# Kernel optimization log

Measured on AMD Instinct MI355X. Metric: run time of the kernel, lower is better.

The kernel has to match this reference:

```python
import jax, jax.numpy as jnp
import numpy as np

B, T, F = 32, 64, 128          # batch, time_steps, input_dim
H = 8                           # feat_dim (GRU hidden, MHA embed)
NH, HD = 4, 2                   # num_heads, head_dim
HID = 32                        # hidden_dim (out_proj out-features)


def setup_inputs() -> dict:
    key = jax.random.key(0)
    ks = jax.random.split(key, 16)
    s = 0.1
    inp = {
        'x': jax.random.normal(ks[0], (B, T, F), jnp.float32),
        # input_proj: Linear(F, F)
        'Wp': jax.random.normal(ks[1], (F, F), jnp.float32) * s,
        'bp': jax.random.normal(ks[2], (F,), jnp.float32) * s,
        # per-feature GRU weights stacked over F (input size 1 -> squeeze)
        'W_ih': jax.random.normal(ks[3], (F, 3 * H), jnp.float32) * s,
        'b_ih': jax.random.normal(ks[4], (F, 3 * H), jnp.float32) * s,
        'W_hh': jax.random.normal(ks[5], (F, 3 * H, H), jnp.float32) * s,
        'b_hh': jax.random.normal(ks[6], (F, 3 * H), jnp.float32) * s,
        # shared MultiheadAttention (embed=H, heads=NH)
        'in_w': jax.random.normal(ks[7], (3 * H, H), jnp.float32) * s,
        'in_b': jax.random.normal(ks[8], (3 * H,), jnp.float32) * s,
        'ow': jax.random.normal(ks[9], (H, H), jnp.float32) * s,
        'ob': jax.random.normal(ks[10], (H,), jnp.float32) * s,
        # out_proj: Linear(F*H, HID)
        'Wout': jax.random.normal(ks[11], (HID, F * H), jnp.float32) * s,
        'bout': jax.random.normal(ks[12], (HID,), jnp.float32) * s,
    }
    return inp


def _forward(x, Wp, bp, W_ih, b_ih, W_hh, b_hh, in_w, in_b, ow, ob, Wout, bout):
    xp = x @ Wp.T + bp                               # [B,T,F] input_proj

    # ---- batched per-feature GRU (vectorized over B and F, scan over T) ----
    def step(h, x_t):                                # h [B,F,H], x_t [B,F]
        gx = x_t[..., None] * W_ih + b_ih            # [B,F,3H]
        gh = jnp.einsum('bfh,fgh->bfg', h, W_hh) + b_hh
        r = jax.nn.sigmoid(gx[..., :H] + gh[..., :H])
        z = jax.nn.sigmoid(gx[..., H:2 * H] + gh[..., H:2 * H])
        n = jnp.tanh(gx[..., 2 * H:] + r * gh[..., 2 * H:])
        h_new = (1.0 - z) * n + z * h
        return h_new, h_new

    h0 = jnp.zeros((x.shape[0], F, H), x.dtype)
    _, hs = jax.lax.scan(step, h0, jnp.moveaxis(xp, 1, 0))   # [T,B,F,H]
    out = jnp.moveaxis(hs, 0, 1)                              # [B,T,F,H]

    # ---- shared MHA over time, batched across (B, F) ----
    seq = out.transpose(0, 2, 1, 3)                           # [B,F,T,H]
    qkv = seq @ in_w.T + in_b                                 # [B,F,T,3H]
    q, k, v = jnp.split(qkv, 3, axis=-1)
    def heads(t):  # [B,F,T,H] -> [B,F,T,NH,HD]
        return t.reshape(t.shape[:-1] + (NH, HD))
    q, k, v = heads(q), heads(k), heads(v)
    scale = 1.0 / np.sqrt(HD)
    scores = jnp.einsum('bfqnd,bfknd->bfnqk', q, k) * scale   # [B,F,NH,T,T]
    w = jax.nn.softmax(scores, axis=-1)
    ctx = jnp.einsum('bfnqk,bfknd->bfqnd', w, v)
    ctx = ctx.reshape(ctx.shape[:2] + (ctx.shape[2], H))      # [B,F,T,H]
    attn_out = ctx @ ow.T + ob                                # [B,F,T,H]
    attention = attn_out.transpose(0, 2, 1, 3)                # [B,T,F,H]

    # ---- flatten GRU outputs and project ----
    y = out.reshape(out.shape[0], out.shape[1], F * H) @ Wout.T + bout  # [B,T,HID]
    return y, attention


def reference(x, Wp, bp, W_ih, b_ih, W_hh, b_hh, in_w, in_b, ow, ob, Wout, bout):
    return _forward(x, Wp, bp, W_ih, b_ih, W_hh, b_hh, in_w, in_b, ow, ob, Wout, bout)
```

## Files before the change

kernel.cpp:

```cpp
#include <hip/hip_runtime.h>


namespace {
constexpr int Bb = 32, Tt = 64, Ff = 128, Hh = 8, HIDh = 32;
constexpr int G3H = 24;
constexpr int XS_STRIDE = 130;
constexpr int XP_OFF = Tt * XS_STRIDE;
constexpr int SMEM_AB = XP_OFF + 8 * 65;
constexpr float L2E = 1.44269504088896340736f;
}

__device__ __forceinline__ float rcp_(float x) {
#if __has_builtin(__builtin_amdgcn_rcpf)
  return __builtin_amdgcn_rcpf(x);
#else
  return 1.0f / x;
#endif
}
__device__ __forceinline__ float exp2_(float x) {
#if __has_builtin(__builtin_amdgcn_exp2f)
  return __builtin_amdgcn_exp2f(x);
#else
  return exp2f(x);
#endif
}

__global__ __launch_bounds__(256) void k_gruproj(
    const float* __restrict__ x, const float* __restrict__ Wp, const float* __restrict__ bp,
    const float* __restrict__ W_ih, const float* __restrict__ b_ih,
    const float* __restrict__ W_hh, const float* __restrict__ b_hh,
    float* __restrict__ outp) {
  __shared__ float smem[SMEM_AB];
  const int tid = threadIdx.x;
  const int blk = blockIdx.x;
  const int b = blk >> 4;
  const int f0 = (blk & 15) * 8;
  const int lane = tid & 63;
  const int w = tid >> 6;

  {
    const float2* xb = (const float2*)(x + b * Tt * Ff);
    for (int i = tid; i < Tt * Ff / 2; i += 256) {
      int row = i >> 6, col2 = i & 63;
      *(float2*)&smem[row * XS_STRIDE + col2 * 2] = xb[i];
    }
  }
  __syncthreads();
  {
    const int t = lane;
    const int fA = f0 + w, fB = f0 + w + 4;
    float acc0 = bp[fA], acc1 = bp[fB];
    const float* wA = Wp + fA * Ff;
    const float* wB = Wp + fB * Ff;
    const float* xr = &smem[t * XS_STRIDE];
#pragma unroll 8
    for (int k = 0; k < Ff; k += 2) {
      float2 xv = *(const float2*)&xr[k];
      acc0 = fmaf(xv.x, wA[k], acc0); acc0 = fmaf(xv.y, wA[k + 1], acc0);
      acc1 = fmaf(xv.x, wB[k], acc1); acc1 = fmaf(xv.y, wB[k + 1], acc1);
    }
    smem[XP_OFF + w * 65 + t] = acc0;
    smem[XP_OFF + (w + 4) * 65 + t] = acc1;
  }
  __syncthreads();
  if (tid >= 64) return;

  {
    const int g = tid >> 3, j = tid & 7;
    const int f = f0 + g;
    const float* wb = W_hh + (f * G3H + j) * Hh;
    const float nL = -L2E, S2 = 2.0f * L2E;
    float w0s[8], w1s[8], w2s[8];
#pragma unroll
    for (int h = 0; h < 8; ++h) {
      w0s[h] = wb[h] * nL;
      w1s[h] = wb[64 + h] * nL;
      w2s[h] = wb[128 + h] * S2;
    }
    const float wi0s = W_ih[f * G3H + j] * nL;
    const float wi1s = W_ih[f * G3H + 8 + j] * nL;
    const float wi2s = W_ih[f * G3H + 16 + j] * S2;
    const float bias_r = (b_ih[f * G3H + j] + b_hh[f * G3H + j]) * nL;
    const float bias_z = (b_ih[f * G3H + 8 + j] + b_hh[f * G3H + 8 + j]) * nL;
    const float bi2s = b_ih[f * G3H + 16 + j] * S2;
    const float bh2s = b_hh[f * G3H + 16 + j] * S2;
    float hall[8];
#pragma unroll
    for (int h = 0; h < 8; ++h) hall[h] = 0.f;
    const int base = tid & 56;
    float* outb = outp + ((b * Ff + f) * Tt) * Hh + j;
    const float* xps = &smem[XP_OFF + g * 65];
    for (int t = 0; t < Tt; ++t) {
      float xt = xps[t];
      float a0 = bias_r, a1 = bias_z, a2 = bh2s;
#pragma unroll
      for (int h = 0; h < 8; ++h) {
        a0 = fmaf(hall[h], w0s[h], a0);
        a1 = fmaf(hall[h], w1s[h], a1);
        a2 = fmaf(hall[h], w2s[h], a2);
      }
      float r = rcp_(1.0f + exp2_(fmaf(xt, wi0s, a0)));
      float z = rcp_(1.0f + exp2_(fmaf(xt, wi1s, a1)));
      float narg = fmaf(r, a2, fmaf(xt, wi2s, bi2s));
      float n = fmaf(-2.0f, rcp_(exp2_(narg) + 1.0f), 1.0f);
      float hn = fmaf(z, hall[j] - n, n);
      outb[t * Hh] = hn;
#pragma unroll
      for (int h = 0; h < 8; ++h) hall[h] = __shfl(hn, base + h, 64);
    }
  }
}

__global__ __launch_bounds__(64) void k_mha(
    const float* __restrict__ outp, const float* __restrict__ in_w,
    const float* __restrict__ in_b, const float* __restrict__ ow,
    const float* __restrict__ ob, float* __restrict__ attn) {
  __shared__ float kvs[4 * 130];
  __shared__ float vvs[4 * 130];
  __shared__ float qs[64 * 10];
  __shared__ float cs[64 * 10];
  const int blk = blockIdx.x;
  const int b = blk >> 7, f = blk & 127;
  const int t = threadIdx.x;

  const float4* src = (const float4*)(outp + blk * (Tt * Hh));
  float4 r0 = src[t * 2], r1 = src[t * 2 + 1];
  float sq[8] = {r0.x, r0.y, r0.z, r0.w, r1.x, r1.y, r1.z, r1.w};
  constexpr float SCL = 0.70710678118654752f * L2E;
  float qv[8], ka[8], va[8];
#pragma unroll
  for (int jj = 0; jj < 8; ++jj) {
    float aq = in_b[jj], ak = in_b[8 + jj], av = in_b[16 + jj];
#pragma unroll
    for (int h = 0; h < 8; ++h) {
      aq = fmaf(sq[h], in_w[jj * 8 + h], aq);
      ak = fmaf(sq[h], in_w[(8 + jj) * 8 + h], ak);
      av = fmaf(sq[h], in_w[(16 + jj) * 8 + h], av);
    }
    qv[jj] = aq * SCL; ka[jj] = ak; va[jj] = av;
  }
#pragma unroll
  for (int n = 0; n < 4; ++n) {
    *(float2*)&qs[t * 10 + 2 * n] = make_float2(qv[2 * n], qv[2 * n + 1]);
    *(float2*)&kvs[n * 130 + 2 * t] = make_float2(ka[2 * n], ka[2 * n + 1]);
    *(float2*)&vvs[n * 130 + 2 * t] = make_float2(va[2 * n], va[2 * n + 1]);
  }
  __syncthreads();

  const int n = t & 3, qq = t >> 2;
  float q0[4], q1[4];
#pragma unroll
  for (int i = 0; i < 4; ++i) {
    float2 qp = *(const float2*)&qs[(qq + 16 * i) * 10 + 2 * n];
    q0[i] = qp.x; q1[i] = qp.y;
  }
  float ps[4], c0[4], c1[4];
#pragma unroll
  for (int i = 0; i < 4; ++i) { ps[i] = 0.f; c0[i] = 0.f; c1[i] = 0.f; }
#pragma unroll 4
  for (int kt = 0; kt < Tt; ++kt) {
    float2 kf = *(const float2*)&kvs[n * 130 + 2 * kt];
    float2 vf = *(const float2*)&vvs[n * 130 + 2 * kt];
#pragma unroll
    for (int i = 0; i < 4; ++i) {
      float s = fmaf(q0[i], kf.x, q1[i] * kf.y);
      float p = exp2_(s);
      ps[i] += p;
      c0[i] = fmaf(p, vf.x, c0[i]);
      c1[i] = fmaf(p, vf.y, c1[i]);
    }
  }
#pragma unroll
  for (int i = 0; i < 4; ++i) {
    float inv = rcp_(ps[i]);
    *(float2*)&cs[(qq + 16 * i) * 10 + 2 * n] = make_float2(c0[i] * inv, c1[i] * inv);
  }
  __syncthreads();

  const float4* owp = (const float4*)(ow + n * 16);
  float4 wv0 = owp[0], wv1 = owp[1], wv2 = owp[2], wv3 = owp[3];
  const float ob0 = ob[2 * n], ob1 = ob[2 * n + 1];
#pragma unroll
  for (int i = 0; i < 4; ++i) {
    int row = qq + 16 * i;
    float2 cp0 = *(const float2*)&cs[row * 10 + 0];
    float2 cp1 = *(const float2*)&cs[row * 10 + 2];
    float2 cp2 = *(const float2*)&cs[row * 10 + 4];
    float2 cp3 = *(const float2*)&cs[row * 10 + 6];
    float o0 = ob0, o1 = ob1;
    o0 = fmaf(cp0.x, wv0.x, o0); o0 = fmaf(cp0.y, wv0.y, o0);
    o0 = fmaf(cp1.x, wv0.z, o0); o0 = fmaf(cp1.y, wv0.w, o0);
    o0 = fmaf(cp2.x, wv1.x, o0); o0 = fmaf(cp2.y, wv1.y, o0);
    o0 = fmaf(cp3.x, wv1.z, o0); o0 = fmaf(cp3.y, wv1.w, o0);
    o1 = fmaf(cp0.x, wv2.x, o1); o1 = fmaf(cp0.y, wv2.y, o1);
    o1 = fmaf(cp1.x, wv2.z, o1); o1 = fmaf(cp1.y, wv2.w, o1);
    o1 = fmaf(cp2.x, wv3.x, o1); o1 = fmaf(cp2.y, wv3.y, o1);
    o1 = fmaf(cp3.x, wv3.z, o1); o1 = fmaf(cp3.y, wv3.w, o1);
    *(float2*)&attn[((b * Tt + row) * Ff + f) * Hh + 2 * n] = make_float2(o0, o1);
  }
}

__global__ __launch_bounds__(128) void k_outproj(
    const float* __restrict__ outp, const float* __restrict__ Wout,
    const float* __restrict__ bout, float* __restrict__ y) {
  constexpr int TT = 8;
  int blk = blockIdx.x;
  int b = blk >> 3;
  int t0 = (blk & 7) * TT;
  int tid = threadIdx.x;
  int oq = tid >> 4;
  int fc = tid & 15;
  float acc[TT][4];
#pragma unroll
  for (int tt = 0; tt < TT; ++tt)
#pragma unroll
    for (int od = 0; od < 4; ++od) acc[tt][od] = 0.f;
#pragma unroll
  for (int ff = 0; ff < 8; ++ff) {
    int f = fc * 8 + ff;
    const float4* rb = (const float4*)(outp + ((b * Ff + f) * Tt + t0) * Hh);
    float4 rv[16];
#pragma unroll
    for (int i = 0; i < 16; ++i) rv[i] = rb[i];
#pragma unroll
    for (int od = 0; od < 4; ++od) {
      int o = oq * 4 + od;
      const float4* wbp = (const float4*)(Wout + o * (Ff * Hh) + f * Hh);
      float4 wa = wbp[0], wc = wbp[1];
#pragma unroll
      for (int tt = 0; tt < TT; ++tt) {
        float4 ra = rv[tt * 2], rc = rv[tt * 2 + 1];
        float s = acc[tt][od];
        s = fmaf(ra.x, wa.x, s); s = fmaf(ra.y, wa.y, s);
        s = fmaf(ra.z, wa.z, s); s = fmaf(ra.w, wa.w, s);
        s = fmaf(rc.x, wc.x, s); s = fmaf(rc.y, wc.y, s);
        s = fmaf(rc.z, wc.z, s); s = fmaf(rc.w, wc.w, s);
        acc[tt][od] = s;
      }
    }
  }
#pragma unroll
  for (int tt = 0; tt < TT; ++tt)
#pragma unroll
    for (int od = 0; od < 4; ++od) {
      float v = acc[tt][od];
      v += __shfl_xor(v, 1, 16);
      v += __shfl_xor(v, 2, 16);
      v += __shfl_xor(v, 4, 16);
      v += __shfl_xor(v, 8, 16);
      acc[tt][od] = v;
    }
#pragma unroll
  for (int tt = 0; tt < TT; ++tt) {
    if (fc == tt) {
#pragma unroll
      for (int od = 0; od < 4; ++od) {
        int o = oq * 4 + od;
        y[(b * Tt + t0 + tt) * HIDh + o] = acc[tt][od] + bout[o];
      }
    }
  }
}

extern "C" void kernel_launch(void* const* d_in, const int* in_sizes, int n_in,
                              void* d_out, int out_size, void* d_ws, size_t ws_size,
                              hipStream_t stream) {
  (void)in_sizes; (void)n_in; (void)out_size; (void)ws_size;
  const float* x    = (const float*)d_in[0];
  const float* Wp   = (const float*)d_in[1];
  const float* bp   = (const float*)d_in[2];
  const float* W_ih = (const float*)d_in[3];
  const float* b_ih = (const float*)d_in[4];
  const float* W_hh = (const float*)d_in[5];
  const float* b_hh = (const float*)d_in[6];
  const float* in_w = (const float*)d_in[7];
  const float* in_b = (const float*)d_in[8];
  const float* ow   = (const float*)d_in[9];
  const float* ob   = (const float*)d_in[10];
  const float* Wout = (const float*)d_in[11];
  const float* bout = (const float*)d_in[12];

  float* y    = (float*)d_out;
  float* attn = (float*)d_out + Bb * Tt * HIDh;
  float* outp = (float*)d_ws;

  hipLaunchKernelGGL(k_gruproj, dim3(Bb * (Ff / 8)), dim3(256), 0, stream,
                     x, Wp, bp, W_ih, b_ih, W_hh, b_hh, outp);
  hipLaunchKernelGGL(k_mha, dim3(Bb * Ff), dim3(64), 0, stream,
                     outp, in_w, in_b, ow, ob, attn);
  hipLaunchKernelGGL(k_outproj, dim3(Bb * (Tt / 8)), dim3(128), 0, stream,
                     outp, Wout, bout, y);
}
```

Measured before the change: 64.31 us.

## Split input projection from GRU, merge MHA and out-projection into one launch

Moves the input projection out of the GRU kernel into its own kernel over all (b,t) rows, so the GRU kernel runs with 64-thread blocks and no longer carries 192 idle threads through the serial recurrence. Fuses the MHA and out-projection kernels into one launch: MHA blocks handle two (b,f) pairs each and the out-projection work is appended as extra blocks. Pads the K/V shared-memory layout to float4 per key. This trades an extra global round trip for xp and a new launch against better GRU occupancy and overlap between the MHA and out-projection work.

```diff
diff --git a/kernel.cpp b/kernel.cpp
--- a/kernel.cpp
+++ b/kernel.cpp
@@ -4,10 +4,12 @@
 namespace {
 constexpr int Bb = 32, Tt = 64, Ff = 128, Hh = 8, HIDh = 32;
 constexpr int G3H = 24;
-constexpr int XS_STRIDE = 130;
-constexpr int XP_OFF = Tt * XS_STRIDE;
-constexpr int SMEM_AB = XP_OFF + 8 * 65;
 constexpr float L2E = 1.44269504088896340736f;
+constexpr int KV4 = 0;
+constexpr int VV4 = 1040;
+constexpr int QS  = 2080;
+constexpr int CS  = 2720;
+constexpr int HALF = 3360;
 }
 
 __device__ __forceinline__ float rcp_(float x) {
@@ -25,238 +27,228 @@
 #endif
 }
 
-__global__ __launch_bounds__(256) void k_gruproj(
-    const float* __restrict__ x, const float* __restrict__ Wp, const float* __restrict__ bp,
-    const float* __restrict__ W_ih, const float* __restrict__ b_ih,
-    const float* __restrict__ W_hh, const float* __restrict__ b_hh,
-    float* __restrict__ outp) {
-  __shared__ float smem[SMEM_AB];
+__global__ __launch_bounds__(256) void k_inproj(
+    const float* __restrict__ x, const float* __restrict__ Wp,
+    const float* __restrict__ bp, float* __restrict__ xp) {
+  __shared__ float xs[2][128];
+  const int r0 = blockIdx.x * 2;
+  const int rr = threadIdx.x >> 7;
+  const int f = threadIdx.x & 127;
+  xs[rr][f] = x[(r0 + rr) * Ff + f];
+  __syncthreads();
+  float acc = bp[f];
+  const float4* wr = (const float4*)(Wp + f * Ff);
+  const float* xr = xs[rr];
+#pragma unroll 8
+  for (int k4 = 0; k4 < Ff / 4; ++k4) {
+    float4 w = wr[k4];
+    float4 xv = *(const float4*)&xr[k4 * 4];
+    acc = fmaf(xv.x, w.x, acc);
+    acc = fmaf(xv.y, w.y, acc);
+    acc = fmaf(xv.z, w.z, acc);
+    acc = fmaf(xv.w, w.w, acc);
+  }
+  xp[(r0 + rr) * Ff + f] = acc;
+}
+
+__global__ __launch_bounds__(64) void k_gru(
+    const float* __restrict__ xp, const float* __restrict__ W_ih,
+    const float* __restrict__ b_ih, const float* __restrict__ W_hh,
+    const float* __restrict__ b_hh, float* __restrict__ outp) {
+  __shared__ float xs[8][65];
   const int tid = threadIdx.x;
   const int blk = blockIdx.x;
   const int b = blk >> 4;
   const int f0 = (blk & 15) * 8;
-  const int lane = tid & 63;
-  const int w = tid >> 6;
-
-  {
-    const float2* xb = (const float2*)(x + b * Tt * Ff);
-    for (int i = tid; i < Tt * Ff / 2; i += 256) {
-      int row = i >> 6, col2 = i & 63;
-      *(float2*)&smem[row * XS_STRIDE + col2 * 2] = xb[i];
-    }
-  }
+  for (int i = tid; i < Tt * 8; i += 64)
+    xs[i & 7][i >> 3] = xp[(b * Tt + (i >> 3)) * Ff + f0 + (i & 7)];
+  const int g = tid >> 3, j = tid & 7;
+  const int f = f0 + g;
+  const float* wb = W_hh + (f * G3H + j) * Hh;
+  const float nL = -L2E, S2 = 2.0f * L2E;
+  float w0s[8], w1s[8], w2s[8];
+#pragma unroll
+  for (int h = 0; h < 8; ++h) {
+    w0s[h] = wb[h] * nL;
+    w1s[h] = wb[64 + h] * nL;
+    w2s[h] = wb[128 + h] * S2;
+  }
+  const float wi0s = W_ih[f * G3H + j] * nL;
+  const float wi1s = W_ih[f * G3H + 8 + j] * nL;
+  const float wi2s = W_ih[f * G3H + 16 + j] * S2;
+  const float bias_r = (b_ih[f * G3H + j] + b_hh[f * G3H + j]) * nL;
+  const float bias_z = (b_ih[f * G3H + 8 + j] + b_hh[f * G3H + 8 + j]) * nL;
+  const float bi2s = b_ih[f * G3H + 16 + j] * S2;
+  const float bh2s = b_hh[f * G3H + 16 + j] * S2;
+  float hall[8];
+#pragma unroll
+  for (int h = 0; h < 8; ++h) hall[h] = 0.f;
+  const int base = tid & 56;
+  float* outb = outp + ((b * Ff + f) * Tt) * Hh + j;
+  const float* xps = &xs[g][0];
   __syncthreads();
-  {
-    const int t = lane;
-    const int fA = f0 + w, fB = f0 + w + 4;
-    float acc0 = bp[fA], acc1 = bp[fB];
-    const float* wA = Wp + fA * Ff;
-    const float* wB = Wp + fB * Ff;
-    const float* xr = &smem[t * XS_STRIDE];
-#pragma unroll 8
-    for (int k = 0; k < Ff; k += 2) {
-      float2 xv = *(const float2*)&xr[k];
-      acc0 = fmaf(xv.x, wA[k], acc0); acc0 = fmaf(xv.y, wA[k + 1], acc0);
-      acc1 = fmaf(xv.x, wB[k], acc1); acc1 = fmaf(xv.y, wB[k + 1], acc1);
-    }
-    smem[XP_OFF + w * 65 + t] = acc0;
-    smem[XP_OFF + (w + 4) * 65 + t] = acc1;
-  }
-  __syncthreads();
-  if (tid >= 64) return;
-
-  {
-    const int g = tid >> 3, j = tid & 7;
-    const int f = f0 + g;
-    const float* wb = W_hh + (f * G3H + j) * Hh;
-    const float nL = -L2E, S2 = 2.0f * L2E;
-    float w0s[8], w1s[8], w2s[8];
+  for (int t = 0; t < Tt; ++t) {
+    float xt = xps[t];
+    float a0 = bias_r, a1 = bias_z, a2 = bh2s;
 #pragma unroll
     for (int h = 0; h < 8; ++h) {
-      w0s[h] = wb[h] * nL;
-      w1s[h] = wb[64 + h] * nL;
-      w2s[h] = wb[128 + h] * S2;
-    }
-    const float wi0s = W_ih[f * G3H + j] * nL;
-    const float wi1s = W_ih[f * G3H + 8 + j] * nL;
-    const float wi2s = W_ih[f * G3H + 16 + j] * S2;
-    const float bias_r = (b_ih[f * G3H + j] + b_hh[f * G3H + j]) * nL;
-    const float bias_z = (b_ih[f * G3H + 8 + j] + b_hh[f * G3H + 8 + j]) * nL;
-    const float bi2s = b_ih[f * G3H + 16 + j] * S2;
-    const float bh2s = b_hh[f * G3H + 16 + j] * S2;
-    float hall[8];
-#pragma unroll
-    for (int h = 0; h < 8; ++h) hall[h] = 0.f;
-    const int base = tid & 56;
-    float* outb = outp + ((b * Ff + f) * Tt) * Hh + j;
-    const float* xps = &smem[XP_OFF + g * 65];
-    for (int t = 0; t < Tt; ++t) {
-      float xt = xps[t];
-      float a0 = bias_r, a1 = bias_z, a2 = bh2s;
-#pragma unroll
-      for (int h = 0; h < 8; ++h) {
-        a0 = fmaf(hall[h], w0s[h], a0);
-        a1 = fmaf(hall[h], w1s[h], a1);
-        a2 = fmaf(hall[h], w2s[h], a2);
-      }
-      float r = rcp_(1.0f + exp2_(fmaf(xt, wi0s, a0)));
-      float z = rcp_(1.0f + exp2_(fmaf(xt, wi1s, a1)));
-      float narg = fmaf(r, a2, fmaf(xt, wi2s, bi2s));
-      float n = fmaf(-2.0f, rcp_(exp2_(narg) + 1.0f), 1.0f);
-      float hn = fmaf(z, hall[j] - n, n);
-      outb[t * Hh] = hn;
-#pragma unroll
-      for (int h = 0; h < 8; ++h) hall[h] = __shfl(hn, base + h, 64);
-    }
-  }
-}
-
-__global__ __launch_bounds__(64) void k_mha(
+      a0 = fmaf(hall[h], w0s[h], a0);
+      a1 = fmaf(hall[h], w1s[h], a1);
+      a2 = fmaf(hall[h], w2s[h], a2);
+    }
+    float r = rcp_(1.0f + exp2_(fmaf(xt, wi0s, a0)));
+    float z = rcp_(1.0f + exp2_(fmaf(xt, wi1s, a1)));
+    float narg = fmaf(r, a2, fmaf(xt, wi2s, bi2s));
+    float n = fmaf(-2.0f, rcp_(exp2_(narg) + 1.0f), 1.0f);
+    float hn = fmaf(z, hall[j] - n, n);
+    outb[t * Hh] = hn;
+#pragma unroll
+    for (int h = 0; h < 8; ++h) hall[h] = __shfl(hn, base + h, 64);
+  }
+}
+
+__global__ __launch_bounds__(128) void k_mha_outproj(
     const float* __restrict__ outp, const float* __restrict__ in_w,
     const float* __restrict__ in_b, const float* __restrict__ ow,
-    const float* __restrict__ ob, float* __restrict__ attn) {
-  __shared__ float kvs[4 * 130];
-  __shared__ float vvs[4 * 130];
-  __shared__ float qs[64 * 10];
-  __shared__ float cs[64 * 10];
-  const int blk = blockIdx.x;
-  const int b = blk >> 7, f = blk & 127;
-  const int t = threadIdx.x;
-
-  const float4* src = (const float4*)(outp + blk * (Tt * Hh));
-  float4 r0 = src[t * 2], r1 = src[t * 2 + 1];
-  float sq[8] = {r0.x, r0.y, r0.z, r0.w, r1.x, r1.y, r1.z, r1.w};
-  constexpr float SCL = 0.70710678118654752f * L2E;
-  float qv[8], ka[8], va[8];
-#pragma unroll
-  for (int jj = 0; jj < 8; ++jj) {
-    float aq = in_b[jj], ak = in_b[8 + jj], av = in_b[16 + jj];
-#pragma unroll
-    for (int h = 0; h < 8; ++h) {
-      aq = fmaf(sq[h], in_w[jj * 8 + h], aq);
-      ak = fmaf(sq[h], in_w[(8 + jj) * 8 + h], ak);
-      av = fmaf(sq[h], in_w[(16 + jj) * 8 + h], av);
-    }
-    qv[jj] = aq * SCL; ka[jj] = ak; va[jj] = av;
-  }
-#pragma unroll
-  for (int n = 0; n < 4; ++n) {
-    *(float2*)&qs[t * 10 + 2 * n] = make_float2(qv[2 * n], qv[2 * n + 1]);
-    *(float2*)&kvs[n * 130 + 2 * t] = make_float2(ka[2 * n], ka[2 * n + 1]);
-    *(float2*)&vvs[n * 130 + 2 * t] = make_float2(va[2 * n], va[2 * n + 1]);
-  }
-  __syncthreads();
-
-  const int n = t & 3, qq = t >> 2;
-  float q0[4], q1[4];
-#pragma unroll
-  for (int i = 0; i < 4; ++i) {
-    float2 qp = *(const float2*)&qs[(qq + 16 * i) * 10 + 2 * n];
-    q0[i] = qp.x; q1[i] = qp.y;
-  }
-  float ps[4], c0[4], c1[4];
-#pragma unroll
-  for (int i = 0; i < 4; ++i) { ps[i] = 0.f; c0[i] = 0.f; c1[i] = 0.f; }
+    const float* __restrict__ ob, const float* __restrict__ Wout,
+    const float* __restrict__ bout, float* __restrict__ attn,
+    float* __restrict__ y) {
+  __shared__ float smem[2 * HALF];
+  const int tid = threadIdx.x;
+  if (blockIdx.x < 2048) {
+    const int pair = blockIdx.x * 2 + (tid >> 6);
+    const int b = pair >> 7, f = pair & 127;
+    const int t = tid & 63;
+    float* sm = &smem[(tid >> 6) * HALF];
+    const float4* src = (const float4*)(outp + pair * (Tt * Hh));
+    float4 r0 = src[t * 2], r1 = src[t * 2 + 1];
+    float sq[8] = {r0.x, r0.y, r0.z, r0.w, r1.x, r1.y, r1.z, r1.w};
+    constexpr float SCL = 0.70710678118654752f * L2E;
+    float qv[8], ka[8], va[8];
+#pragma unroll
+    for (int jj = 0; jj < 8; ++jj) {
+      float aq = in_b[jj], ak = in_b[8 + jj], av = in_b[16 + jj];
+#pragma unroll
+      for (int h = 0; h < 8; ++h) {
+        aq = fmaf(sq[h], in_w[jj * 8 + h], aq);
+        ak = fmaf(sq[h], in_w[(8 + jj) * 8 + h], ak);
+        av = fmaf(sq[h], in_w[(16 + jj) * 8 + h], av);
+      }
+      qv[jj] = aq * SCL; ka[jj] = ak; va[jj] = av;
+    }
+#pragma unroll
+    for (int n = 0; n < 4; ++n) {
+      *(float2*)&sm[QS + t * 10 + 2 * n] = make_float2(qv[2 * n], qv[2 * n + 1]);
+      *(float4*)&sm[KV4 + (n * 65 + t) * 4] = make_float4(ka[2 * n], ka[2 * n + 1], 0.f, 0.f);
+      *(float4*)&sm[VV4 + (n * 65 + t) * 4] = make_float4(va[2 * n], va[2 * n + 1], 0.f, 0.f);
+    }
+    __syncthreads();
+    const int n = t & 3, qq = t >> 2;
+    float q0[4], q1[4];
+#pragma unroll
+    for (int i = 0; i < 4; ++i) {
+      float2 qp = *(const float2*)&sm[QS + (qq + 16 * i) * 10 + 2 * n];
+      q0[i] = qp.x; q1[i] = qp.y;
+    }
+    float ps[4], c0[4], c1[4];
+#pragma unroll
+    for (int i = 0; i < 4; ++i) { ps[i] = 0.f; c0[i] = 0.f; c1[i] = 0.f; }
 #pragma unroll 4
-  for (int kt = 0; kt < Tt; ++kt) {
-    float2 kf = *(const float2*)&kvs[n * 130 + 2 * kt];
-    float2 vf = *(const float2*)&vvs[n * 130 + 2 * kt];
+    for (int kt = 0; kt < Tt; ++kt) {
+      float4 kf = *(const float4*)&sm[KV4 + (n * 65 + kt) * 4];
+      float4 vf = *(const float4*)&sm[VV4 + (n * 65 + kt) * 4];
+#pragma unroll
+      for (int i = 0; i < 4; ++i) {
+        float s = fmaf(q0[i], kf.x, q1[i] * kf.y);
+        float p = exp2_(s);
+        ps[i] += p;
+        c0[i] = fmaf(p, vf.x, c0[i]);
+        c1[i] = fmaf(p, vf.y, c1[i]);
+      }
+    }
 #pragma unroll
     for (int i = 0; i < 4; ++i) {
-      float s = fmaf(q0[i], kf.x, q1[i] * kf.y);
-      float p = exp2_(s);
-      ps[i] += p;
-      c0[i] = fmaf(p, vf.x, c0[i]);
-      c1[i] = fmaf(p, vf.y, c1[i]);
-    }
-  }
-#pragma unroll
-  for (int i = 0; i < 4; ++i) {
-    float inv = rcp_(ps[i]);
-    *(float2*)&cs[(qq + 16 * i) * 10 + 2 * n] = make_float2(c0[i] * inv, c1[i] * inv);
-  }
-  __syncthreads();
-
-  const float4* owp = (const float4*)(ow + n * 16);
-  float4 wv0 = owp[0], wv1 = owp[1], wv2 = owp[2], wv3 = owp[3];
-  const float ob0 = ob[2 * n], ob1 = ob[2 * n + 1];
-#pragma unroll
-  for (int i = 0; i < 4; ++i) {
-    int row = qq + 16 * i;
-    float2 cp0 = *(const float2*)&cs[row * 10 + 0];
-    float2 cp1 = *(const float2*)&cs[row * 10 + 2];
-    float2 cp2 = *(const float2*)&cs[row * 10 + 4];
-    float2 cp3 = *(const float2*)&cs[row * 10 + 6];
-    float o0 = ob0, o1 = ob1;
-    o0 = fmaf(cp0.x, wv0.x, o0); o0 = fmaf(cp0.y, wv0.y, o0);
-    o0 = fmaf(cp1.x, wv0.z, o0); o0 = fmaf(cp1.y, wv0.w, o0);
-    o0 = fmaf(cp2.x, wv1.x, o0); o0 = fmaf(cp2.y, wv1.y, o0);
-    o0 = fmaf(cp3.x, wv1.z, o0); o0 = fmaf(cp3.y, wv1.w, o0);
-    o1 = fmaf(cp0.x, wv2.x, o1); o1 = fmaf(cp0.y, wv2.y, o1);
-    o1 = fmaf(cp1.x, wv2.z, o1); o1 = fmaf(cp1.y, wv2.w, o1);
-    o1 = fmaf(cp2.x, wv3.x, o1); o1 = fmaf(cp2.y, wv3.y, o1);
-    o1 = fmaf(cp3.x, wv3.z, o1); o1 = fmaf(cp3.y, wv3.w, o1);
-    *(float2*)&attn[((b * Tt + row) * Ff + f) * Hh + 2 * n] = make_float2(o0, o1);
-  }
-}
-
-__global__ __launch_bounds__(128) void k_outproj(
-    const float* __restrict__ outp, const float* __restrict__ Wout,
-    const float* __restrict__ bout, float* __restrict__ y) {
-  constexpr int TT = 8;
-  int blk = blockIdx.x;
-  int b = blk >> 3;
-  int t0 = (blk & 7) * TT;
-  int tid = threadIdx.x;
-  int oq = tid >> 4;
-  int fc = tid & 15;
-  float acc[TT][4];
-#pragma unroll
-  for (int tt = 0; tt < TT; ++tt)
-#pragma unroll
-    for (int od = 0; od < 4; ++od) acc[tt][od] = 0.f;
-#pragma unroll
-  for (int ff = 0; ff < 8; ++ff) {
-    int f = fc * 8 + ff;
-    const float4* rb = (const float4*)(outp + ((b * Ff + f) * Tt + t0) * Hh);
-    float4 rv[16];
-#pragma unroll
-    for (int i = 0; i < 16; ++i) rv[i] = rb[i];
-#pragma unroll
-    for (int od = 0; od < 4; ++od) {
-      int o = oq * 4 + od;
-      const float4* wbp = (const float4*)(Wout + o * (Ff * Hh) + f * Hh);
-      float4 wa = wbp[0], wc = wbp[1];
-#pragma unroll
-      for (int tt = 0; tt < TT; ++tt) {
-        float4 ra = rv[tt * 2], rc = rv[tt * 2 + 1];
-        float s = acc[tt][od];
-        s = fmaf(ra.x, wa.x, s); s = fmaf(ra.y, wa.y, s);
-        s = fmaf(ra.z, wa.z, s); s = fmaf(ra.w, wa.w, s);
-        s = fmaf(rc.x, wc.x, s); s = fmaf(rc.y, wc.y, s);
-        s = fmaf(rc.z, wc.z, s); s = fmaf(rc.w, wc.w, s);
-        acc[tt][od] = s;
-      }
-    }
-  }
-#pragma unroll
-  for (int tt = 0; tt < TT; ++tt)
-#pragma unroll
-    for (int od = 0; od < 4; ++od) {
-      float v = acc[tt][od];
-      v += __shfl_xor(v, 1, 16);
-      v += __shfl_xor(v, 2, 16);
-      v += __shfl_xor(v, 4, 16);
-      v += __shfl_xor(v, 8, 16);
-      acc[tt][od] = v;
-    }
-#pragma unroll
-  for (int tt = 0; tt < TT; ++tt) {
-    if (fc == tt) {
+      float inv = rcp_(ps[i]);
+      *(float2*)&sm[CS + (qq + 16 * i) * 10 + 2 * n] =
+          make_float2(c0[i] * inv, c1[i] * inv);
+    }
+    __syncthreads();
+    const float4* owp = (const float4*)(ow + n * 16);
+    float4 wv0 = owp[0], wv1 = owp[1], wv2 = owp[2], wv3 = owp[3];
+    const float ob0 = ob[2 * n], ob1 = ob[2 * n + 1];
+#pragma unroll
+    for (int i = 0; i < 4; ++i) {
+      int row = qq + 16 * i;
+      float2 cp0 = *(const float2*)&sm[CS + row * 10 + 0];
+      float2 cp1 = *(const float2*)&sm[CS + row * 10 + 2];
+      float2 cp2 = *(const float2*)&sm[CS + row * 10 + 4];
+      float2 cp3 = *(const float2*)&sm[CS + row * 10 + 6];
+      float o0 = ob0, o1 = ob1;
+      o0 = fmaf(cp0.x, wv0.x, o0); o0 = fmaf(cp0.y, wv0.y, o0);
+      o0 = fmaf(cp1.x, wv0.z, o0); o0 = fmaf(cp1.y, wv0.w, o0);
+      o0 = fmaf(cp2.x, wv1.x, o0); o0 = fmaf(cp2.y, wv1.y, o0);
+      o0 = fmaf(cp3.x, wv1.z, o0); o0 = fmaf(cp3.y, wv1.w, o0);
+      o1 = fmaf(cp0.x, wv2.x, o1); o1 = fmaf(cp0.y, wv2.y, o1);
+      o1 = fmaf(cp1.x, wv2.z, o1); o1 = fmaf(cp1.y, wv2.w, o1);
+      o1 = fmaf(cp2.x, wv3.x, o1); o1 = fmaf(cp2.y, wv3.y, o1);
+      o1 = fmaf(cp3.x, wv3.z, o1); o1 = fmaf(cp3.y, wv3.w, o1);
+      *(float2*)&attn[((b * Tt + row) * Ff + f) * Hh + 2 * n] = make_float2(o0, o1);
+    }
+  } else {
+    constexpr int TT = 8;
+    const int blk = blockIdx.x - 2048;
+    const int b = blk >> 3;
+    const int t0 = (blk & 7) * TT;
+    const int oq = tid >> 4;
+    const int fc = tid & 15;
+    float acc[TT][4];
+#pragma unroll
+    for (int tt = 0; tt < TT; ++tt)
+#pragma unroll
+      for (int od = 0; od < 4; ++od) acc[tt][od] = 0.f;
+#pragma unroll
+    for (int ff = 0; ff < 8; ++ff) {
+      int f = fc * 8 + ff;
+      const float4* rb = (const float4*)(outp + ((b * Ff + f) * Tt + t0) * Hh);
+      float4 rv[16];
+#pragma unroll
+      for (int i = 0; i < 16; ++i) rv[i] = rb[i];
 #pragma unroll
       for (int od = 0; od < 4; ++od) {
         int o = oq * 4 + od;
-        y[(b * Tt + t0 + tt) * HIDh + o] = acc[tt][od] + bout[o];
+        const float4* wbp = (const float4*)(Wout + o * (Ff * Hh) + f * Hh);
+        float4 wa = wbp[0], wc = wbp[1];
+#pragma unroll
+        for (int tt = 0; tt < TT; ++tt) {
+          float4 ra = rv[tt * 2], rc = rv[tt * 2 + 1];
+          float s = acc[tt][od];
+          s = fmaf(ra.x, wa.x, s); s = fmaf(ra.y, wa.y, s);
+          s = fmaf(ra.z, wa.z, s); s = fmaf(ra.w, wa.w, s);
+          s = fmaf(rc.x, wc.x, s); s = fmaf(rc.y, wc.y, s);
+          s = fmaf(rc.z, wc.z, s); s = fmaf(rc.w, wc.w, s);
+          acc[tt][od] = s;
+        }
+      }
+    }
+#pragma unroll
+    for (int tt = 0; tt < TT; ++tt)
+#pragma unroll
+      for (int od = 0; od < 4; ++od) {
+        float v = acc[tt][od];
+        v += __shfl_xor(v, 1, 16);
+        v += __shfl_xor(v, 2, 16);
+        v += __shfl_xor(v, 4, 16);
+        v += __shfl_xor(v, 8, 16);
+        acc[tt][od] = v;
+      }
+#pragma unroll
+    for (int tt = 0; tt < TT; ++tt) {
+      if (fc == tt) {
+#pragma unroll
+        for (int od = 0; od < 4; ++od) {
+          int o = oq * 4 + od;
+          y[(b * Tt + t0 + tt) * HIDh + o] = acc[tt][od] + bout[o];
+        }
       }
     }
   }
@@ -282,12 +274,12 @@
 
   float* y    = (float*)d_out;
   float* attn = (float*)d_out + Bb * Tt * HIDh;
-  float* outp = (float*)d_ws;
-
-  hipLaunchKernelGGL(k_gruproj, dim3(Bb * (Ff / 8)), dim3(256), 0, stream,
-                     x, Wp, bp, W_ih, b_ih, W_hh, b_hh, outp);
-  hipLaunchKernelGGL(k_mha, dim3(Bb * Ff), dim3(64), 0, stream,
-                     outp, in_w, in_b, ow, ob, attn);
-  hipLaunchKernelGGL(k_outproj, dim3(Bb * (Tt / 8)), dim3(128), 0, stream,
-                     outp, Wout, bout, y);
-}
+  float* xp   = (float*)d_ws;
+  float* outp = (float*)d_ws + Bb * Tt * Ff;
+
+  hipLaunchKernelGGL(k_inproj, dim3(Bb * Tt / 2), dim3(256), 0, stream, x, Wp, bp, xp);
+  hipLaunchKernelGGL(k_gru, dim3(Bb * (Ff / 8)), dim3(64), 0, stream,
+                     xp, W_ih, b_ih, W_hh, b_hh, outp);
+  hipLaunchKernelGGL(k_mha_outproj, dim3(2304), dim3(128), 0, stream,
+                     outp, in_w, in_b, ow, ob, Wout, bout, attn, y);
+}
```

Measured after the change: 78.83 us. +22.6%, slower.

## Merge MHA and output projection into one launch with wave-local attention

Applied to the files above, without the earlier changes.

Combines the attention kernel and the output-projection kernel into a single launch. The first 1024 blocks run four (b,f) attention problems per block, one per wave, and the last 128 blocks run two output-projection tiles each. Attention now uses only wave-local LDS regions, so the block barriers become lgkmcnt waits. K and V are stored split-component so the inner loop loads float4 runs, and each thread computes a full row of the output projection, writing it as float4 stores. This removes one launch and the barrier cost, but it depends on wave-synchronous LDS visibility within a 64-lane wave.

```diff
diff --git a/kernel.cpp b/kernel.cpp
--- a/kernel.cpp
+++ b/kernel.cpp
@@ -4,10 +4,12 @@
 namespace {
 constexpr int Bb = 32, Tt = 64, Ff = 128, Hh = 8, HIDh = 32;
 constexpr int G3H = 24;
+constexpr float L2E = 1.44269504088896340736f;
 constexpr int XS_STRIDE = 130;
 constexpr int XP_OFF = Tt * XS_STRIDE;
 constexpr int SMEM_AB = XP_OFF + 8 * 65;
-constexpr float L2E = 1.44269504088896340736f;
+constexpr int KK0 = 0, KK1 = 272, VV0 = 544, VV1 = 816, QS = 1088;
+constexpr int WREG = 1728;
 }
 
 __device__ __forceinline__ float rcp_(float x) {
@@ -111,152 +113,159 @@
   }
 }
 
-__global__ __launch_bounds__(64) void k_mha(
+#define MHA_STEP(K0C, K1C, V0C, V1C)                         \
+  {                                                          \
+    _Pragma("unroll") for (int i = 0; i < 4; ++i) {          \
+      float s = fmaf(q0[i], K0C, q1[i] * K1C);               \
+      float p = exp2_(s);                                    \
+      ps[i] += p;                                            \
+      c0[i] = fmaf(p, V0C, c0[i]);                           \
+      c1[i] = fmaf(p, V1C, c1[i]);                           \
+    }                                                        \
+  }
+
+__global__ __launch_bounds__(256) void k_mha_outproj(
     const float* __restrict__ outp, const float* __restrict__ in_w,
     const float* __restrict__ in_b, const float* __restrict__ ow,
-    const float* __restrict__ ob, float* __restrict__ attn) {
-  __shared__ float kvs[4 * 130];
-  __shared__ float vvs[4 * 130];
-  __shared__ float qs[64 * 10];
-  __shared__ float cs[64 * 10];
-  const int blk = blockIdx.x;
-  const int b = blk >> 7, f = blk & 127;
-  const int t = threadIdx.x;
-
-  const float4* src = (const float4*)(outp + blk * (Tt * Hh));
-  float4 r0 = src[t * 2], r1 = src[t * 2 + 1];
-  float sq[8] = {r0.x, r0.y, r0.z, r0.w, r1.x, r1.y, r1.z, r1.w};
-  constexpr float SCL = 0.70710678118654752f * L2E;
-  float qv[8], ka[8], va[8];
-#pragma unroll
-  for (int jj = 0; jj < 8; ++jj) {
-    float aq = in_b[jj], ak = in_b[8 + jj], av = in_b[16 + jj];
-#pragma unroll
-    for (int h = 0; h < 8; ++h) {
-      aq = fmaf(sq[h], in_w[jj * 8 + h], aq);
-      ak = fmaf(sq[h], in_w[(8 + jj) * 8 + h], ak);
-      av = fmaf(sq[h], in_w[(16 + jj) * 8 + h], av);
-    }
-    qv[jj] = aq * SCL; ka[jj] = ak; va[jj] = av;
-  }
-#pragma unroll
-  for (int n = 0; n < 4; ++n) {
-    *(float2*)&qs[t * 10 + 2 * n] = make_float2(qv[2 * n], qv[2 * n + 1]);
-    *(float2*)&kvs[n * 130 + 2 * t] = make_float2(ka[2 * n], ka[2 * n + 1]);
-    *(float2*)&vvs[n * 130 + 2 * t] = make_float2(va[2 * n], va[2 * n + 1]);
-  }
-  __syncthreads();
-
-  const int n = t & 3, qq = t >> 2;
-  float q0[4], q1[4];
-#pragma unroll
-  for (int i = 0; i < 4; ++i) {
-    float2 qp = *(const float2*)&qs[(qq + 16 * i) * 10 + 2 * n];
-    q0[i] = qp.x; q1[i] = qp.y;
-  }
-  float ps[4], c0[4], c1[4];
-#pragma unroll
-  for (int i = 0; i < 4; ++i) { ps[i] = 0.f; c0[i] = 0.f; c1[i] = 0.f; }
-#pragma unroll 4
-  for (int kt = 0; kt < Tt; ++kt) {
-    float2 kf = *(const float2*)&kvs[n * 130 + 2 * kt];
-    float2 vf = *(const float2*)&vvs[n * 130 + 2 * kt];
+    const float* __restrict__ ob, const float* __restrict__ Wout,
+    const float* __restrict__ bout, float* __restrict__ attn,
+    float* __restrict__ y) {
+  __shared__ float smem[4 * WREG];
+  const int tid = threadIdx.x;
+  if (blockIdx.x < 1024) {
+    const int wv = tid >> 6;
+    const int t = tid & 63;
+    const int pair = blockIdx.x * 4 + wv;
+    const int b = pair >> 7, f = pair & 127;
+    float* sm = &smem[wv * WREG];
+
+    const float4* src = (const float4*)(outp + pair * (Tt * Hh));
+    float4 r0 = src[t * 2], r1 = src[t * 2 + 1];
+    float sq[8] = {r0.x, r0.y, r0.z, r0.w, r1.x, r1.y, r1.z, r1.w};
+    constexpr float SCL = 0.70710678118654752f * L2E;
+    float qv[8], ka[8], va[8];
+#pragma unroll
+    for (int jj = 0; jj < 8; ++jj) {
+      float aq = in_b[jj], ak = in_b[8 + jj], av = in_b[16 + jj];
+#pragma unroll
+      for (int h = 0; h < 8; ++h) {
+        aq = fmaf(sq[h], in_w[jj * 8 + h], aq);
+        ak = fmaf(sq[h], in_w[(8 + jj) * 8 + h], ak);
+        av = fmaf(sq[h], in_w[(16 + jj) * 8 + h], av);
+      }
+      qv[jj] = aq * SCL; ka[jj] = ak; va[jj] = av;
+    }
+#pragma unroll
+    for (int n = 0; n < 4; ++n) {
+      *(float2*)&sm[QS + t * 10 + 2 * n] = make_float2(qv[2 * n], qv[2 * n + 1]);
+      sm[KK0 + n * 68 + t] = ka[2 * n];
+      sm[KK1 + n * 68 + t] = ka[2 * n + 1];
+      sm[VV0 + n * 68 + t] = va[2 * n];
+      sm[VV1 + n * 68 + t] = va[2 * n + 1];
+    }
+    asm volatile("s_waitcnt lgkmcnt(0)" ::: "memory");
+
+    const int n = t >> 4, qq = t & 15;
+    float q0[4], q1[4];
 #pragma unroll
     for (int i = 0; i < 4; ++i) {
-      float s = fmaf(q0[i], kf.x, q1[i] * kf.y);
-      float p = exp2_(s);
-      ps[i] += p;
-      c0[i] = fmaf(p, vf.x, c0[i]);
-      c1[i] = fmaf(p, vf.y, c1[i]);
-    }
-  }
-#pragma unroll
-  for (int i = 0; i < 4; ++i) {
-    float inv = rcp_(ps[i]);
-    *(float2*)&cs[(qq + 16 * i) * 10 + 2 * n] = make_float2(c0[i] * inv, c1[i] * inv);
-  }
-  __syncthreads();
-
-  const float4* owp = (const float4*)(ow + n * 16);
-  float4 wv0 = owp[0], wv1 = owp[1], wv2 = owp[2], wv3 = owp[3];
-  const float ob0 = ob[2 * n], ob1 = ob[2 * n + 1];
-#pragma unroll
-  for (int i = 0; i < 4; ++i) {
-    int row = qq + 16 * i;
-    float2 cp0 = *(const float2*)&cs[row * 10 + 0];
-    float2 cp1 = *(const float2*)&cs[row * 10 + 2];
-    float2 cp2 = *(const float2*)&cs[row * 10 + 4];
-    float2 cp3 = *(const float2*)&cs[row * 10 + 6];
-    float o0 = ob0, o1 = ob1;
-    o0 = fmaf(cp0.x, wv0.x, o0); o0 = fmaf(cp0.y, wv0.y, o0);
-    o0 = fmaf(cp1.x, wv0.z, o0); o0 = fmaf(cp1.y, wv0.w, o0);
-    o0 = fmaf(cp2.x, wv1.x, o0); o0 = fmaf(cp2.y, wv1.y, o0);
-    o0 = fmaf(cp3.x, wv1.z, o0); o0 = fmaf(cp3.y, wv1.w, o0);
-    o1 = fmaf(cp0.x, wv2.x, o1); o1 = fmaf(cp0.y, wv2.y, o1);
-    o1 = fmaf(cp1.x, wv2.z, o1); o1 = fmaf(cp1.y, wv2.w, o1);
-    o1 = fmaf(cp2.x, wv3.x, o1); o1 = fmaf(cp2.y, wv3.y, o1);
-    o1 = fmaf(cp3.x, wv3.z, o1); o1 = fmaf(cp3.y, wv3.w, o1);
-    *(float2*)&attn[((b * Tt + row) * Ff + f) * Hh + 2 * n] = make_float2(o0, o1);
-  }
-}
-
-__global__ __launch_bounds__(128) void k_outproj(
-    const float* __restrict__ outp, const float* __restrict__ Wout,
-    const float* __restrict__ bout, float* __restrict__ y) {
-  constexpr int TT = 8;
-  int blk = blockIdx.x;
-  int b = blk >> 3;
-  int t0 = (blk & 7) * TT;
-  int tid = threadIdx.x;
-  int oq = tid >> 4;
-  int fc = tid & 15;
-  float acc[TT][4];
-#pragma unroll
-  for (int tt = 0; tt < TT; ++tt)
-#pragma unroll
-    for (int od = 0; od < 4; ++od) acc[tt][od] = 0.f;
-#pragma unroll
-  for (int ff = 0; ff < 8; ++ff) {
-    int f = fc * 8 + ff;
-    const float4* rb = (const float4*)(outp + ((b * Ff + f) * Tt + t0) * Hh);
-    float4 rv[16];
-#pragma unroll
-    for (int i = 0; i < 16; ++i) rv[i] = rb[i];
-#pragma unroll
-    for (int od = 0; od < 4; ++od) {
-      int o = oq * 4 + od;
-      const float4* wbp = (const float4*)(Wout + o * (Ff * Hh) + f * Hh);
-      float4 wa = wbp[0], wc = wbp[1];
-#pragma unroll
-      for (int tt = 0; tt < TT; ++tt) {
-        float4 ra = rv[tt * 2], rc = rv[tt * 2 + 1];
-        float s = acc[tt][od];
-        s = fmaf(ra.x, wa.x, s); s = fmaf(ra.y, wa.y, s);
-        s = fmaf(ra.z, wa.z, s); s = fmaf(ra.w, wa.w, s);
-        s = fmaf(rc.x, wc.x, s); s = fmaf(rc.y, wc.y, s);
-        s = fmaf(rc.z, wc.z, s); s = fmaf(rc.w, wc.w, s);
-        acc[tt][od] = s;
-      }
-    }
-  }
-#pragma unroll
-  for (int tt = 0; tt < TT; ++tt)
-#pragma unroll
-    for (int od = 0; od < 4; ++od) {
-      float v = acc[tt][od];
-      v += __shfl_xor(v, 1, 16);
-      v += __shfl_xor(v, 2, 16);
-      v += __shfl_xor(v, 4, 16);
-      v += __shfl_xor(v, 8, 16);
-      acc[tt][od] = v;
-    }
-#pragma unroll
-  for (int tt = 0; tt < TT; ++tt) {
-    if (fc == tt) {
+      float2 qp = *(const float2*)&sm[QS + (qq + 16 * i) * 10 + 2 * n];
+      q0[i] = qp.x; q1[i] = qp.y;
+    }
+    float ps[4], c0[4], c1[4];
+#pragma unroll
+    for (int i = 0; i < 4; ++i) { ps[i] = 0.f; c0[i] = 0.f; c1[i] = 0.f; }
+#pragma unroll 2
+    for (int kt4 = 0; kt4 < Tt; kt4 += 4) {
+      float4 k0 = *(const float4*)&sm[KK0 + n * 68 + kt4];
+      float4 k1 = *(const float4*)&sm[KK1 + n * 68 + kt4];
+      float4 v0 = *(const float4*)&sm[VV0 + n * 68 + kt4];
+      float4 v1 = *(const float4*)&sm[VV1 + n * 68 + kt4];
+      MHA_STEP(k0.x, k1.x, v0.x, v1.x)
+      MHA_STEP(k0.y, k1.y, v0.y, v1.y)
+      MHA_STEP(k0.z, k1.z, v0.z, v1.z)
+      MHA_STEP(k0.w, k1.w, v0.w, v1.w)
+    }
+#pragma unroll
+    for (int i = 0; i < 4; ++i) {
+      float inv = rcp_(ps[i]);
+      *(float2*)&sm[QS + (qq + 16 * i) * 10 + 2 * n] =
+          make_float2(c0[i] * inv, c1[i] * inv);
+    }
+    asm volatile("s_waitcnt lgkmcnt(0)" ::: "memory");
+
+    float2 cp0 = *(const float2*)&sm[QS + t * 10 + 0];
+    float2 cp1 = *(const float2*)&sm[QS + t * 10 + 2];
+    float2 cp2 = *(const float2*)&sm[QS + t * 10 + 4];
+    float2 cp3 = *(const float2*)&sm[QS + t * 10 + 6];
+    float cx[8] = {cp0.x, cp0.y, cp1.x, cp1.y, cp2.x, cp2.y, cp3.x, cp3.y};
+    float o8[8];
+#pragma unroll
+    for (int jj = 0; jj < 8; ++jj) {
+      float a = ob[jj];
+#pragma unroll
+      for (int h = 0; h < 8; ++h) a = fmaf(cx[h], ow[jj * 8 + h], a);
+      o8[jj] = a;
+    }
+    float4* dst = (float4*)(attn + ((b * Tt + t) * Ff + f) * Hh);
+    dst[0] = make_float4(o8[0], o8[1], o8[2], o8[3]);
+    dst[1] = make_float4(o8[4], o8[5], o8[6], o8[7]);
+  } else {
+    constexpr int TT = 8;
+    const int sub = tid >> 7, stid = tid & 127;
+    const int eblk = (blockIdx.x - 1024) * 2 + sub;
+    const int b = eblk >> 3;
+    const int t0 = (eblk & 7) * TT;
+    const int oq = stid >> 4;
+    const int fc = stid & 15;
+    float acc[TT][4];
+#pragma unroll
+    for (int tt = 0; tt < TT; ++tt)
+#pragma unroll
+      for (int od = 0; od < 4; ++od) acc[tt][od] = 0.f;
+#pragma unroll
+    for (int ff = 0; ff < 8; ++ff) {
+      int f = fc * 8 + ff;
+      const float4* rb = (const float4*)(outp + ((b * Ff + f) * Tt + t0) * Hh);
+      float4 rv[16];
+#pragma unroll
+      for (int i = 0; i < 16; ++i) rv[i] = rb[i];
 #pragma unroll
       for (int od = 0; od < 4; ++od) {
         int o = oq * 4 + od;
-        y[(b * Tt + t0 + tt) * HIDh + o] = acc[tt][od] + bout[o];
+        const float4* wbp = (const float4*)(Wout + o * (Ff * Hh) + f * Hh);
+        float4 wa = wbp[0], wc = wbp[1];
+#pragma unroll
+        for (int tt = 0; tt < TT; ++tt) {
+          float4 ra = rv[tt * 2], rc = rv[tt * 2 + 1];
+          float s = acc[tt][od];
+          s = fmaf(ra.x, wa.x, s); s = fmaf(ra.y, wa.y, s);
+          s = fmaf(ra.z, wa.z, s); s = fmaf(ra.w, wa.w, s);
+          s = fmaf(rc.x, wc.x, s); s = fmaf(rc.y, wc.y, s);
+          s = fmaf(rc.z, wc.z, s); s = fmaf(rc.w, wc.w, s);
+          acc[tt][od] = s;
+        }
+      }
+    }
+#pragma unroll
+    for (int tt = 0; tt < TT; ++tt)
+#pragma unroll
+      for (int od = 0; od < 4; ++od) {
+        float v = acc[tt][od];
+        v += __shfl_xor(v, 1, 16);
+        v += __shfl_xor(v, 2, 16);
+        v += __shfl_xor(v, 4, 16);
+        v += __shfl_xor(v, 8, 16);
+        acc[tt][od] = v;
+      }
+#pragma unroll
+    for (int tt = 0; tt < TT; ++tt) {
+      if (fc == tt) {
+#pragma unroll
+        for (int od = 0; od < 4; ++od) {
+          int o = oq * 4 + od;
+          y[(b * Tt + t0 + tt) * HIDh + o] = acc[tt][od] + bout[o];
+        }
       }
     }
   }
@@ -286,8 +295,6 @@
 
   hipLaunchKernelGGL(k_gruproj, dim3(Bb * (Ff / 8)), dim3(256), 0, stream,
                      x, Wp, bp, W_ih, b_ih, W_hh, b_hh, outp);
-  hipLaunchKernelGGL(k_mha, dim3(Bb * Ff), dim3(64), 0, stream,
-                     outp, in_w, in_b, ow, ob, attn);
-  hipLaunchKernelGGL(k_outproj, dim3(Bb * (Tt / 8)), dim3(128), 0, stream,
-                     outp, Wout, bout, y);
-}
+  hipLaunchKernelGGL(k_mha_outproj, dim3(1152), dim3(256), 0, stream,
+                     outp, in_w, in_b, ow, ob, Wout, bout, attn, y);
+}
```

After: 67.84 us. 5.5% more time.
